# Performance work log

Hardware: AMD Instinct MI355X
Metric: run time of the kernel (lower is better)

The kernel has to match this reference:

```python
import jax, jax.numpy as jnp
import numpy as np

N = 100000
EPS = 1e-5


def sage_conv(x, edge_index, w_l, b_l, w_r):
    # PyG SAGEConv (aggr='mean'): out = lin_l(mean_{j in N(i)} x_j) + lin_r(x_i)
    src = edge_index[0]
    tgt = edge_index[1]
    msg = x[src]                                        # [E, d] gather
    agg = jax.ops.segment_sum(msg, tgt, num_segments=N)  # [N, d] scatter-add
    cnt = jax.ops.segment_sum(jnp.ones_like(tgt, dtype=x.dtype), tgt, num_segments=N)
    mean = agg / jnp.maximum(cnt, 1.0)[:, None]
    return mean @ w_l.T + b_l + x @ w_r.T


def batchnorm(h, gamma, beta):
    mu = jnp.mean(h, axis=0)
    var = jnp.var(h, axis=0)  # biased, matches torch BN training normalization
    return (h - mu) * jax.lax.rsqrt(var + EPS) * gamma + beta


def setup_inputs() -> dict:
    key = jax.random.key(0)
    ks = jax.random.split(key, 16)
    d_in, d_h, h1, h2 = 32, 64, 128, 64
    E = 1600000
    inp = {
        "x": jax.random.normal(ks[0], (N, d_in), dtype=jnp.float32),
        "edge_index": jax.random.randint(ks[1], (2, E), 0, N, dtype=jnp.int64),
        # SAGEConv 1 (bias in lin_l only)
        "w_l1": jax.random.normal(ks[2], (d_h, d_in), dtype=jnp.float32) * 0.1,
        "b_l1": jnp.zeros((d_h,), dtype=jnp.float32),
        "w_r1": jax.random.normal(ks[3], (d_h, d_in), dtype=jnp.float32) * 0.1,
        # SAGEConv 2
        "w_l2": jax.random.normal(ks[4], (d_h, d_h), dtype=jnp.float32) * 0.1,
        "b_l2": jnp.zeros((d_h,), dtype=jnp.float32),
        "w_r2": jax.random.normal(ks[5], (d_h, d_h), dtype=jnp.float32) * 0.1,
        # MLP head
        "fc1_w": jax.random.normal(ks[6], (h1, d_h), dtype=jnp.float32) * 0.1,
        "fc1_b": jnp.zeros((h1,), dtype=jnp.float32),
        "bn1_g": jnp.ones((h1,), dtype=jnp.float32),
        "bn1_b": jnp.zeros((h1,), dtype=jnp.float32),
        "fc2_w": jax.random.normal(ks[7], (h2, h1), dtype=jnp.float32) * 0.1,
        "fc2_b": jnp.zeros((h2,), dtype=jnp.float32),
        "bn2_g": jnp.ones((h2,), dtype=jnp.float32),
        "bn2_b": jnp.zeros((h2,), dtype=jnp.float32),
        "fc3_w": jax.random.normal(ks[8], (1, h2), dtype=jnp.float32) * 0.1,
        "fc3_b": jnp.zeros((1,), dtype=jnp.float32),
    }
    return inp


def reference(x, edge_index, w_l1, b_l1, w_r1, w_l2, b_l2, w_r2,
              fc1_w, fc1_b, bn1_g, bn1_b, fc2_w, fc2_b, bn2_g, bn2_b,
              fc3_w, fc3_b):
    h1 = jax.nn.relu(sage_conv(x, edge_index, w_l1, b_l1, w_r1))   # [N, 64]
    h2 = jax.nn.relu(sage_conv(h1, edge_index, w_l2, b_l2, w_r2))  # [N, 64]
    z = jax.nn.relu(batchnorm(h2 @ fc1_w.T + fc1_b, bn1_g, bn1_b))
    z = jax.nn.relu(batchnorm(z @ fc2_w.T + fc2_b, bn2_g, bn2_b))
    out = (z @ fc3_w.T + fc3_b).squeeze(-1)                        # [N]
    return (out, h1, h2)
```

## Files before the change

kernel.cpp:

```cpp
#include <hip/hip_runtime.h>

#define NN 100000
#define EPS 1e-5f

static const size_t OFF_ROWST  = 0;
static const size_t OFF_ROWEN  = 100000;
static const size_t OFF_ADJ    = 200000;
static const size_t OFF_AGG1   = 2886976;
static const size_t OFF_AGG2   = 6086976;
static const size_t OFF_PAIRS  = 2886976;
static const size_t OFF_XB     = 12486976;
static const size_t OFF_Z1     = 0;
static const size_t OFF_H1B    = 14086976;
static const size_t OFF_Z2     = 14086976;
static const size_t OFF_WSPL   = 20487000;
static const size_t OFF_BUKCNT = 20515712;
static const size_t OFF_STATS1 = 20515968;
static const size_t OFF_STATS2 = 20548736;
static const size_t OFF_COEF1  = 20565120;
static const size_t OFF_COEF2  = 20565376;
static const size_t ZERO_START = 20515712;
static const size_t ZERO_INTS  = 49664;

#define NSLOT 128

#define WL1_HI 0
#define WL1_LO 2048
#define WR1_HI 4096
#define WR1_LO 6144
#define WL2_HI 8192
#define WL2_LO 12288
#define WR2_HI 16384
#define WR2_LO 20480
#define F1_HI  24576
#define F1_LO  32768
#define F2_HI  40960
#define F2_LO  49152

#define NBUK 256
#define BSHIFT 9
#define BCAP 10496
#define CHUNK 2048

typedef __attribute__((ext_vector_type(8))) short short8;
typedef __attribute__((ext_vector_type(4))) float f32x4;

#define MFMA_16x16x32(a, b, c) __builtin_amdgcn_mfma_f32_16x16x32_bf16(a, b, c, 0, 0, 0)

__device__ inline unsigned short f2bf(float f) {
  unsigned u = __builtin_bit_cast(unsigned, f);
  unsigned r = (u + 0x7fffu + ((u >> 16) & 1u)) >> 16;
  return (unsigned short)r;
}
__device__ inline float bf2f(unsigned short h) {
  unsigned u = ((unsigned)h) << 16;
  return __builtin_bit_cast(float, u);
}

template<bool BNIN>
__device__ inline void load_split(const float* __restrict__ p,
                                  const float* __restrict__ ca,
                                  const float* __restrict__ cc,
                                  short8& hi, short8& lo) {
  #pragma unroll
  for (int j = 0; j < 8; ++j) {
    float v = p[j];
    if (BNIN) v = fmaxf(v * ca[j] + cc[j], 0.f);
    unsigned short h = f2bf(v);
    hi[j] = (short)h;
    lo[j] = (short)f2bf(v - bf2f(h));
  }
}

struct WsplitArgs {
  const float* src[6];
  unsigned short* dhi[6];
  unsigned short* dlo[6];
  int n[6];
};
__global__ __launch_bounds__(256) void wsplit_k(WsplitArgs a) {
  int m = blockIdx.y;
  int n = a.n[m];
  for (int i = blockIdx.x * 256 + threadIdx.x; i < n; i += gridDim.x * 256) {
    float v = a.src[m][i];
    unsigned short h = f2bf(v);
    a.dhi[m][i] = h;
    a.dlo[m][i] = f2bf(v - bf2f(h));
  }
}

__global__ __launch_bounds__(256) void cvt_bf_k(const float* __restrict__ in,
                                                unsigned short* __restrict__ out,
                                                int n8) {
  int t = blockIdx.x * 256 + threadIdx.x;
  if (t >= n8) return;
  const float4* p = (const float4*)(in + (size_t)t * 8);
  float4 a = p[0], b = p[1];
  ushort4 u0, u1;
  u0.x = f2bf(a.x); u0.y = f2bf(a.y); u0.z = f2bf(a.z); u0.w = f2bf(a.w);
  u1.x = f2bf(b.x); u1.y = f2bf(b.y); u1.z = f2bf(b.z); u1.w = f2bf(b.w);
  ((ushort4*)(out + (size_t)t * 8))[0] = u0;
  ((ushort4*)(out + (size_t)t * 8))[1] = u1;
}

__global__ __launch_bounds__(256) void bpart2_k(const int* __restrict__ ei, int E,
                                                int* __restrict__ bukcnt,
                                                int2* __restrict__ pairs) {
  __shared__ int h[NBUK], wb[NBUK], cur[NBUK];
  int tid = threadIdx.x;
  h[tid] = 0; cur[tid] = 0;
  __syncthreads();
  int lo = blockIdx.x * CHUNK, hi = min(lo + CHUNK, E);
  for (int e = lo + tid; e < hi; e += 256) {
    int t = ei[E + e];
    if ((unsigned)t < NN) atomicAdd(&h[t >> BSHIFT], 1);
  }
  __syncthreads();
  wb[tid] = h[tid] ? atomicAdd(&bukcnt[tid], h[tid]) : 0;
  __syncthreads();
  for (int e = lo + tid; e < hi; e += 256) {
    int s = ei[e], t = ei[E + e];
    if ((unsigned)t >= NN) continue;
    if ((unsigned)s >= NN) s = 0;
    int b = t >> BSHIFT;
    int off = atomicAdd(&cur[b], 1);
    pairs[(size_t)b * BCAP + wb[b] + off] = make_int2(s, t);
  }
}

__global__ __launch_bounds__(256) void bfill2_k(const int2* __restrict__ pairs,
                                                const int* __restrict__ bukcnt,
                                                int* __restrict__ rowstart,
                                                int* __restrict__ rowend,
                                                int* __restrict__ adj) {
  __shared__ int d[512];
  __shared__ int part[256];
  int b = blockIdx.x;
  int t = threadIdx.x;
  int base = b * BCAP, cnt = bukcnt[b];
  d[t] = 0; d[t + 256] = 0;
  __syncthreads();
  for (int p = base + t; p < base + cnt; p += 256)
    atomicAdd(&d[pairs[p].y & 511], 1);
  __syncthreads();
  int d0 = d[2 * t], d1 = d[2 * t + 1];
  part[t] = d0 + d1;
  __syncthreads();
  for (int o = 1; o < 256; o <<= 1) {
    int u = (t >= o) ? part[t - o] : 0;
    __syncthreads();
    part[t] += u;
    __syncthreads();
  }
  int e0 = (t > 0) ? part[t - 1] : 0;
  int e1 = e0 + d0;
  d[2 * t] = e0;
  d[2 * t + 1] = e1;
  int n0 = (b << BSHIFT) + 2 * t;
  if (n0 < NN)     { rowstart[n0]     = base + e0; rowend[n0]     = base + e1; }
  if (n0 + 1 < NN) { rowstart[n0 + 1] = base + e1; rowend[n0 + 1] = base + e1 + d1; }
  __syncthreads();
  for (int p = base + t; p < base + cnt; p += 256) {
    int2 pr = pairs[p];
    int pos = atomicAdd(&d[pr.y & 511], 1);
    adj[base + pos] = pr.x;
  }
}

template<int K>
__global__ __launch_bounds__(256) void aggregate_bf(const unsigned short* __restrict__ xb,
                                                    const int* __restrict__ rowstart,
                                                    const int* __restrict__ rowend,
                                                    const int* __restrict__ adj,
                                                    float* __restrict__ agg) {
  constexpr int GL = K / 4;
  constexpr int NPB = 256 / GL;
  int lg = threadIdx.x & (GL - 1);
  int node = blockIdx.x * NPB + (threadIdx.x / GL);
  if (node >= NN) return;
  int s0 = rowstart[node], s1 = rowend[node];
  float4 a0 = {0,0,0,0}, a1 = {0,0,0,0}, a2 = {0,0,0,0}, a3 = {0,0,0,0};
  int e = s0;
  for (; e + 3 < s1; e += 4) {
    int i0 = adj[e], i1 = adj[e+1], i2 = adj[e+2], i3 = adj[e+3];
    ushort4 u0 = *(const ushort4*)(xb + (size_t)i0 * K + lg * 4);
    ushort4 u1 = *(const ushort4*)(xb + (size_t)i1 * K + lg * 4);
    ushort4 u2 = *(const ushort4*)(xb + (size_t)i2 * K + lg * 4);
    ushort4 u3 = *(const ushort4*)(xb + (size_t)i3 * K + lg * 4);
    a0.x += bf2f(u0.x); a0.y += bf2f(u0.y); a0.z += bf2f(u0.z); a0.w += bf2f(u0.w);
    a1.x += bf2f(u1.x); a1.y += bf2f(u1.y); a1.z += bf2f(u1.z); a1.w += bf2f(u1.w);
    a2.x += bf2f(u2.x); a2.y += bf2f(u2.y); a2.z += bf2f(u2.z); a2.w += bf2f(u2.w);
    a3.x += bf2f(u3.x); a3.y += bf2f(u3.y); a3.z += bf2f(u3.z); a3.w += bf2f(u3.w);
  }
  for (; e < s1; ++e) {
    ushort4 u = *(const ushort4*)(xb + (size_t)adj[e] * K + lg * 4);
    a0.x += bf2f(u.x); a0.y += bf2f(u.y); a0.z += bf2f(u.z); a0.w += bf2f(u.w);
  }
  float inv = 1.0f / fmaxf((float)(s1 - s0), 1.0f);
  float4 r;
  r.x = (a0.x + a1.x + a2.x + a3.x) * inv;
  r.y = (a0.y + a1.y + a2.y + a3.y) * inv;
  r.z = (a0.z + a1.z + a2.z + a3.z) * inv;
  r.w = (a0.w + a1.w + a2.w + a3.w) * inv;
  *(float4*)(agg + (size_t)node * K + lg * 4) = r;
}

template<int K, int C, bool SAGE, bool BNIN, bool RELU, bool BFOUT, bool STATS>
__global__ __launch_bounds__(256) void mfma_dense(const float* __restrict__ inA,
                                                  const float* __restrict__ inB,
                                                  const unsigned short* __restrict__ whiA,
                                                  const unsigned short* __restrict__ wloA,
                                                  const unsigned short* __restrict__ whiB,
                                                  const unsigned short* __restrict__ wloB,
                                                  const float* __restrict__ bias,
                                                  const float* __restrict__ coef,
                                                  float* __restrict__ out,
                                                  unsigned short* __restrict__ outb,
                                                  float* __restrict__ stats) {
  constexpr int KF = K / 32;
  constexpr int KC = K / 8;
  constexpr int SWZ = (KC < 8 ? KC : 8) - 1;
  __shared__ unsigned short swhiA[C * K], swloA[C * K];
  __shared__ unsigned short swhiB[SAGE ? C * K : 8], swloB[SAGE ? C * K : 8];
  __shared__ float ls[STATS ? C : 1], lq[STATS ? C : 1];

  int tid = threadIdx.x;
  for (int i = tid; i < C * KC; i += 256) {
    int col = i / KC, c = i % KC;
    int pos = col * KC + (c ^ (col & SWZ));
    ((short8*)swhiA)[pos] = ((const short8*)whiA)[i];
    ((short8*)swloA)[pos] = ((const short8*)wloA)[i];
    if (SAGE) {
      ((short8*)swhiB)[pos] = ((const short8*)whiB)[i];
      ((short8*)swloB)[pos] = ((const short8*)wloB)[i];
    }
  }
  if (STATS) {
    for (int i = tid; i < C; i += 256) { ls[i] = 0.f; lq[i] = 0.f; }
  }
  __syncthreads();

  int wid  = tid >> 6;
  int lane = tid & 63;
  int row0 = blockIdx.x * 64 + wid * 16;
  int r = lane & 15, g = lane >> 4;
  int arow = row0 + r; if (arow > NN - 1) arow = NN - 1;
  int koff = g * 8;

  short8 ahi[KF], alo[KF];
  short8 a2hi[SAGE ? KF : 1], a2lo[SAGE ? KF : 1];
  #pragma unroll
  for (int kf = 0; kf < KF; ++kf) {
    const float* p = inA + (size_t)arow * K + kf * 32 + koff;
    load_split<BNIN>(p, coef + kf * 32 + koff, coef + K + kf * 32 + koff,
                     ahi[kf], alo[kf]);
  }
  if (SAGE) {
    #pragma unroll
    for (int kf = 0; kf < KF; ++kf) {
      const float* p = inB + (size_t)arow * K + kf * 32 + koff;
      load_split<false>(p, nullptr, nullptr, a2hi[kf], a2lo[kf]);
    }
  }

  #pragma unroll
  for (int cf = 0; cf < C / 16; ++cf) {
    int col = cf * 16 + r;
    float bv = bias[col];
    f32x4 acc = {bv, bv, bv, bv};
    #pragma unroll
    for (int kf = 0; kf < KF; ++kf) {
      int c = kf * 4 + g;
      int pos = col * KC + (c ^ (col & SWZ));
      short8 whi = ((const short8*)swhiA)[pos];
      short8 wlo = ((const short8*)swloA)[pos];
      acc = MFMA_16x16x32(ahi[kf], whi, acc);
      acc = MFMA_16x16x32(ahi[kf], wlo, acc);
      acc = MFMA_16x16x32(alo[kf], whi, acc);
      if (SAGE) {
        short8 vhi = ((const short8*)swhiB)[pos];
        short8 vlo = ((const short8*)swloB)[pos];
        acc = MFMA_16x16x32(a2hi[kf], vhi, acc);
        acc = MFMA_16x16x32(a2hi[kf], vlo, acc);
        acc = MFMA_16x16x32(a2lo[kf], vhi, acc);
      }
    }
    if (STATS) {
      float s = 0.f, q = 0.f;
      #pragma unroll
      for (int j = 0; j < 4; ++j) {
        if (row0 + g * 4 + j < NN) {
          float v = acc[j];
          s += v; q += v * v;
        }
      }
      s += __shfl_xor(s, 16, 64); s += __shfl_xor(s, 32, 64);
      q += __shfl_xor(q, 16, 64); q += __shfl_xor(q, 32, 64);
      if (g == 0) { atomicAdd(&ls[col], s); atomicAdd(&lq[col], q); }
    }
    #pragma unroll
    for (int j = 0; j < 4; ++j) {
      int orow = row0 + g * 4 + j;
      if (orow < NN) {
        float v = acc[j];
        if (RELU) v = fmaxf(v, 0.f);
        out[(size_t)orow * C + col] = v;
        if (BFOUT) outb[(size_t)orow * C + col] = f2bf(v);
      }
    }
  }
  if (STATS) {
    __syncthreads();
    float* sl = stats + (size_t)(blockIdx.x & (NSLOT - 1)) * 2 * C;
    for (int i = tid; i < C; i += 256) {
      atomicAdd(&sl[i], ls[i]);
      atomicAdd(&sl[C + i], lq[i]);
    }
  }
}

__global__ void bncoef(const float* __restrict__ stats, const float* __restrict__ g,
                       const float* __restrict__ b, float* __restrict__ coef, int C) {
  int j = threadIdx.x;
  if (j >= C) return;
  float s = 0.f, q = 0.f;
  for (int sl = 0; sl < NSLOT; ++sl) {
    s += stats[(size_t)sl * 2 * C + j];
    q += stats[(size_t)sl * 2 * C + C + j];
  }
  float mu  = s * (1.0f / NN);
  float var = q * (1.0f / NN) - mu * mu;
  float a = g[j] * rsqrtf(var + EPS);
  coef[j] = a;
  coef[C + j] = b[j] - mu * a;
}

__global__ __launch_bounds__(256) void final_k(const float* __restrict__ z2,
                                               const float* __restrict__ coef,
                                               const float* __restrict__ fc3w,
                                               const float* __restrict__ fc3b,
                                               float* __restrict__ out) {
  int t = blockIdx.x * 256 + threadIdx.x;
  int i = t >> 6;
  int j = t & 63;
  if (i >= NN) return;
  float v = z2[(size_t)i * 64 + j];
  float p = fmaxf(v * coef[j] + coef[64 + j], 0.f) * fc3w[j];
  #pragma unroll
  for (int o = 32; o > 0; o >>= 1) p += __shfl_xor(p, o, 64);
  if (j == 0) out[i] = p + fc3b[0];
}

extern "C" void kernel_launch(void* const* d_in, const int* in_sizes, int n_in,
                              void* d_out, int out_size, void* d_ws, size_t ws_size,
                              hipStream_t stream) {
  const float* x     = (const float*)d_in[0];
  const int*   ei    = (const int*)d_in[1];
  const float* w_l1  = (const float*)d_in[2];
  const float* b_l1  = (const float*)d_in[3];
  const float* w_r1  = (const float*)d_in[4];
  const float* w_l2  = (const float*)d_in[5];
  const float* b_l2  = (const float*)d_in[6];
  const float* w_r2  = (const float*)d_in[7];
  const float* fc1_w = (const float*)d_in[8];
  const float* fc1_b = (const float*)d_in[9];
  const float* bn1_g = (const float*)d_in[10];
  const float* bn1_b = (const float*)d_in[11];
  const float* fc2_w = (const float*)d_in[12];
  const float* fc2_b = (const float*)d_in[13];
  const float* bn2_g = (const float*)d_in[14];
  const float* bn2_b = (const float*)d_in[15];
  const float* fc3_w = (const float*)d_in[16];
  const float* fc3_b = (const float*)d_in[17];

  const int E = in_sizes[1] / 2;

  float* ws       = (float*)d_ws;
  int*   rowstart = (int*)(ws + OFF_ROWST);
  int*   rowend   = (int*)(ws + OFF_ROWEN);
  int*   adj      = (int*)(ws + OFF_ADJ);
  float* agg1     = ws + OFF_AGG1;
  float* agg2     = ws + OFF_AGG2;
  unsigned short* xb  = (unsigned short*)(ws + OFF_XB);
  unsigned short* h1b = (unsigned short*)(ws + OFF_H1B);
  float* z1       = ws + OFF_Z1;
  float* z2       = ws + OFF_Z2;
  int*   bukcnt   = (int*)(ws + OFF_BUKCNT);
  float* stats1   = ws + OFF_STATS1;
  float* stats2   = ws + OFF_STATS2;
  float* coef1    = ws + OFF_COEF1;
  float* coef2    = ws + OFF_COEF2;
  int2*  pairs    = (int2*)(ws + OFF_PAIRS);
  unsigned short* wspl = (unsigned short*)(ws + OFF_WSPL);

  float* outv = (float*)d_out;
  float* h1   = outv + NN;
  float* h2   = h1 + (size_t)NN * 64;

  hipMemsetAsync(ws + ZERO_START, 0, ZERO_INTS * sizeof(float), stream);

  WsplitArgs wa;
  wa.src[0] = w_l1;  wa.dhi[0] = wspl + WL1_HI; wa.dlo[0] = wspl + WL1_LO; wa.n[0] = 64 * 32;
  wa.src[1] = w_r1;  wa.dhi[1] = wspl + WR1_HI; wa.dlo[1] = wspl + WR1_LO; wa.n[1] = 64 * 32;
  wa.src[2] = w_l2;  wa.dhi[2] = wspl + WL2_HI; wa.dlo[2] = wspl + WL2_LO; wa.n[2] = 64 * 64;
  wa.src[3] = w_r2;  wa.dhi[3] = wspl + WR2_HI; wa.dlo[3] = wspl + WR2_LO; wa.n[3] = 64 * 64;
  wa.src[4] = fc1_w; wa.dhi[4] = wspl + F1_HI;  wa.dlo[4] = wspl + F1_LO;  wa.n[4] = 128 * 64;
  wa.src[5] = fc2_w; wa.dhi[5] = wspl + F2_HI;  wa.dlo[5] = wspl + F2_LO;  wa.n[5] = 64 * 128;
  wsplit_k<<<dim3(8, 6), 256, 0, stream>>>(wa);

  cvt_bf_k<<<(NN * 32 / 8 + 255) / 256, 256, 0, stream>>>(x, xb, NN * 32 / 8);

  const int NCH = (E + CHUNK - 1) / CHUNK;
  bpart2_k<<<NCH, 256, 0, stream>>>(ei, E, bukcnt, pairs);
  bfill2_k<<<NBUK, 256, 0, stream>>>(pairs, bukcnt, rowstart, rowend, adj);

  const int MB = (NN + 63) / 64;

  aggregate_bf<32><<<(NN + 31) / 32, 256, 0, stream>>>(xb, rowstart, rowend, adj, agg1);
  mfma_dense<32, 64, true, false, true, true, false><<<MB, 256, 0, stream>>>(
      agg1, x, wspl + WL1_HI, wspl + WL1_LO, wspl + WR1_HI, wspl + WR1_LO,
      b_l1, nullptr, h1, h1b, nullptr);

  aggregate_bf<64><<<(NN + 15) / 16, 256, 0, stream>>>(h1b, rowstart, rowend, adj, agg2);
  mfma_dense<64, 64, true, false, true, false, false><<<MB, 256, 0, stream>>>(
      agg2, h1, wspl + WL2_HI, wspl + WL2_LO, wspl + WR2_HI, wspl + WR2_LO,
      b_l2, nullptr, h2, nullptr, nullptr);

  mfma_dense<64, 128, false, false, false, false, true><<<MB, 256, 0, stream>>>(
      h2, nullptr, wspl + F1_HI, wspl + F1_LO, nullptr, nullptr,
      fc1_b, nullptr, z1, nullptr, stats1);
  bncoef<<<1, 128, 0, stream>>>(stats1, bn1_g, bn1_b, coef1, 128);

  mfma_dense<128, 64, false, true, false, false, true><<<MB, 256, 0, stream>>>(
      z1, nullptr, wspl + F2_HI, wspl + F2_LO, nullptr, nullptr,
      fc2_b, coef1, z2, nullptr, stats2);
  bncoef<<<1, 64, 0, stream>>>(stats2, bn2_g, bn2_b, coef2, 64);

  final_k<<<(NN * 64 + 255) / 256, 256, 0, stream>>>(z2, coef2, fc3_w, fc3_b, outv);
}
```

Baseline: 245.7 us.

## Replace atomic bucket partition with deterministic histogram-scan-scatter and packed pairs

```diff
diff --git a/kernel.cpp b/kernel.cpp
--- a/kernel.cpp
+++ b/kernel.cpp
@@ -19,8 +19,9 @@
 static const size_t OFF_STATS2 = 20548736;
 static const size_t OFF_COEF1  = 20565120;
 static const size_t OFF_COEF2  = 20565376;
-static const size_t ZERO_START = 20515712;
-static const size_t ZERO_INTS  = 49664;
+static const size_t OFF_BHIST  = 20565504;
+static const size_t ZERO_START = 20515968;
+static const size_t ZERO_INTS  = 49152;
 
 #define NSLOT 128
 
@@ -103,12 +104,11 @@
   ((ushort4*)(out + (size_t)t * 8))[1] = u1;
 }
 
-__global__ __launch_bounds__(256) void bpart2_k(const int* __restrict__ ei, int E,
-                                                int* __restrict__ bukcnt,
-                                                int2* __restrict__ pairs) {
-  __shared__ int h[NBUK], wb[NBUK], cur[NBUK];
+__global__ __launch_bounds__(256) void hista_k(const int* __restrict__ ei, int E,
+                                               int* __restrict__ blockhist) {
+  __shared__ int h[NBUK];
   int tid = threadIdx.x;
-  h[tid] = 0; cur[tid] = 0;
+  h[tid] = 0;
   __syncthreads();
   int lo = blockIdx.x * CHUNK, hi = min(lo + CHUNK, E);
   for (int e = lo + tid; e < hi; e += 256) {
@@ -116,19 +116,53 @@
     if ((unsigned)t < NN) atomicAdd(&h[t >> BSHIFT], 1);
   }
   __syncthreads();
-  wb[tid] = h[tid] ? atomicAdd(&bukcnt[tid], h[tid]) : 0;
-  __syncthreads();
+  blockhist[(size_t)blockIdx.x * NBUK + tid] = h[tid];
+}
+
+__global__ __launch_bounds__(256) void scanb_k(int* __restrict__ blockhist, int nch,
+                                               int* __restrict__ bukcnt) {
+  __shared__ int sh[256];
+  int b = blockIdx.x, t = threadIdx.x;
+  int run = 0;
+  for (int base = 0; base < nch; base += 256) {
+    int c = base + t;
+    int v = (c < nch) ? blockhist[(size_t)c * NBUK + b] : 0;
+    sh[t] = v;
+    __syncthreads();
+    for (int o = 1; o < 256; o <<= 1) {
+      int u = (t >= o) ? sh[t - o] : 0;
+      __syncthreads();
+      sh[t] += u;
+      __syncthreads();
+    }
+    if (c < nch) blockhist[(size_t)c * NBUK + b] = run + sh[t] - v;
+    int tot = sh[255];
+    __syncthreads();
+    run += tot;
+  }
+  if (t == 0) bukcnt[b] = run;
+}
+
+__global__ __launch_bounds__(256) void scat_k(const int* __restrict__ ei, int E,
+                                              const int* __restrict__ blockhist,
+                                              unsigned* __restrict__ pairs) {
+  __shared__ int wb[NBUK], cur[NBUK];
+  int tid = threadIdx.x;
+  wb[tid] = blockhist[(size_t)blockIdx.x * NBUK + tid];
+  cur[tid] = 0;
+  __syncthreads();
+  int lo = blockIdx.x * CHUNK, hi = min(lo + CHUNK, E);
   for (int e = lo + tid; e < hi; e += 256) {
     int s = ei[e], t = ei[E + e];
     if ((unsigned)t >= NN) continue;
     if ((unsigned)s >= NN) s = 0;
     int b = t >> BSHIFT;
     int off = atomicAdd(&cur[b], 1);
-    pairs[(size_t)b * BCAP + wb[b] + off] = make_int2(s, t);
-  }
-}
-
-__global__ __launch_bounds__(256) void bfill2_k(const int2* __restrict__ pairs,
+    pairs[(size_t)b * BCAP + wb[b] + off] = ((unsigned)s << 9) | (unsigned)(t & 511);
+  }
+}
+
+__global__ __launch_bounds__(256) void bfill2_k(const unsigned* __restrict__ pairs,
                                                 const int* __restrict__ bukcnt,
                                                 int* __restrict__ rowstart,
                                                 int* __restrict__ rowend,
@@ -141,7 +175,7 @@
   d[t] = 0; d[t + 256] = 0;
   __syncthreads();
   for (int p = base + t; p < base + cnt; p += 256)
-    atomicAdd(&d[pairs[p].y & 511], 1);
+    atomicAdd(&d[pairs[p] & 511], 1);
   __syncthreads();
   int d0 = d[2 * t], d1 = d[2 * t + 1];
   part[t] = d0 + d1;
@@ -161,9 +195,9 @@
   if (n0 + 1 < NN) { rowstart[n0 + 1] = base + e1; rowend[n0 + 1] = base + e1 + d1; }
   __syncthreads();
   for (int p = base + t; p < base + cnt; p += 256) {
-    int2 pr = pairs[p];
-    int pos = atomicAdd(&d[pr.y & 511], 1);
-    adj[base + pos] = pr.x;
+    unsigned pr = pairs[p];
+    int pos = atomicAdd(&d[pr & 511], 1);
+    adj[base + pos] = (int)(pr >> 9);
   }
 }
 
@@ -390,7 +424,8 @@
   float* stats2   = ws + OFF_STATS2;
   float* coef1    = ws + OFF_COEF1;
   float* coef2    = ws + OFF_COEF2;
-  int2*  pairs    = (int2*)(ws + OFF_PAIRS);
+  unsigned* pairs = (unsigned*)(ws + OFF_PAIRS);
+  int*   bhist    = (int*)(ws + OFF_BHIST);
   unsigned short* wspl = (unsigned short*)(ws + OFF_WSPL);
 
   float* outv = (float*)d_out;
@@ -411,7 +446,9 @@
   cvt_bf_k<<<(NN * 32 / 8 + 255) / 256, 256, 0, stream>>>(x, xb, NN * 32 / 8);
 
   const int NCH = (E + CHUNK - 1) / CHUNK;
-  bpart2_k<<<NCH, 256, 0, stream>>>(ei, E, bukcnt, pairs);
+  hista_k<<<NCH, 256, 0, stream>>>(ei, E, bhist);
+  scanb_k<<<NBUK, 256, 0, stream>>>(bhist, NCH, bukcnt);
+  scat_k<<<NCH, 256, 0, stream>>>(ei, E, bhist, pairs);
   bfill2_k<<<NBUK, 256, 0, stream>>>(pairs, bukcnt, rowstart, rowend, adj);
 
   const int MB = (NN + 63) / 64;
```

New measurement: 241.9 us. No clear change (-1.6%).
